# Performance work log

Measured on AMD Instinct MI355X. Metric: run time of the kernel, lower is better.

The kernel has to match this reference:

```python
import jax, jax.numpy as jnp
import numpy as np

B, N, IN, HID, OUT = 32, 128, 64, 128, 64
_off = np.ones((N, N)) - np.eye(N)
RECV, SEND = np.where(_off)  # rel_rec one-hot rows -> receiver idx, rel_send -> sender idx
E = N * (N - 1)


def _bn(x, g, b):
    # BatchNorm1d in training mode over flattened (B*M, C), eps=1e-5, biased var
    c = x.shape[-1]
    xf = x.reshape(-1, c)
    m = xf.mean(0)
    v = ((xf - m) ** 2).mean(0)
    return (((xf - m) / jnp.sqrt(v + 1e-5)) * g + b).reshape(x.shape)


def _mlp(x, W1, b1, W2, b2, g, b):
    h = jax.nn.silu(x @ W1 + b1)
    h = jax.nn.silu(h @ W2 + b2)
    return _bn(h, g, b)


def setup_inputs() -> dict:
    key = jax.random.key(0)
    ks = jax.random.split(key, 8)
    p = lambda k, s: jax.random.normal(k, s, dtype=jnp.float32) * 0.05
    return {
        "node_feature": jax.random.normal(ks[0], (B, N, IN), dtype=jnp.float32),
        "nodes_mask": jnp.ones((B, N), dtype=jnp.float32),
        "edges_mask": jnp.ones((B, E), dtype=jnp.float32),
        "eW1": p(ks[1], (2 * IN, HID)), "eb1": jnp.full((HID,), 0.1, jnp.float32),
        "eW2": p(ks[2], (HID, HID)), "eb2": jnp.full((HID,), 0.1, jnp.float32),
        "eg": jnp.ones((HID,), jnp.float32), "ebt": jnp.zeros((HID,), jnp.float32),
        "nW1": p(ks[3], (HID, HID)), "nb1": jnp.full((HID,), 0.1, jnp.float32),
        "nW2": p(ks[4], (HID, HID)), "nb2": jnp.full((HID,), 0.1, jnp.float32),
        "ng": jnp.ones((HID,), jnp.float32), "nbt": jnp.zeros((HID,), jnp.float32),
        "mW1": p(ks[5], (IN + HID, HID)), "mb1": jnp.full((HID,), 0.1, jnp.float32),
        "mW2": p(ks[6], (HID, OUT)), "mb2": jnp.full((OUT,), 0.1, jnp.float32),
        "mg": jnp.ones((OUT,), jnp.float32), "mbt": jnp.zeros((OUT,), jnp.float32),
        "t_nodes": 0, "t_edges": 0,
    }


def reference(node_feature, nodes_mask, edges_mask,
              eW1, eb1, eW2, eb2, eg, ebt,
              nW1, nb1, nW2, nb2, ng, nbt,
              mW1, mb1, mW2, mb2, mg, mbt,
              t_nodes, t_edges):
    # edge_model: rel_send/rel_rec one-hot matmuls == gathers
    senders = node_feature[:, SEND, :]    # [B,E,IN]
    receivers = node_feature[:, RECV, :]  # [B,E,IN]
    ef = jnp.concatenate([senders, receivers], axis=-1)  # [B,E,2*IN]
    # skip_first_edge_type=True, edge_types=2 -> only edge_nn[1], norm=1.0
    em = edges_mask[:, :, None]
    msg = _mlp(ef, eW1, eb1, eW2, eb2, eg, ebt) * em  # [B,E,HID]
    mij = msg / 1.0
    out = mij * em       # attention=False
    mij_m = mij * em
    # node_model: rel_rec.T matmul == scatter-sum over receivers, then / N
    incoming = jnp.zeros((B, N, HID), msg.dtype).at[:, RECV, :].add(out) / N
    incoming = _mlp(incoming, nW1, nb1, nW2, nb2, ng, nbt) * nodes_mask[:, :, None]
    nef = jnp.concatenate([node_feature, incoming], axis=-1)  # [B,N,IN+HID]
    out_node = _mlp(nef, mW1, mb1, mW2, mb2, mg, mbt) * nodes_mask[:, :, None]
    return (out_node, mij_m)
```

## Files before the change

kernel.cpp:

```cpp
#include <hip/hip_runtime.h>
#include <hip/hip_bf16.h>

#define BB    32
#define NNODE 128
#define INF   64
#define HIDF  128
#define OUTF  64
#define EE    (NNODE*(NNODE-1))
#define TILES 127
#define NBLK_EDGE (BB*TILES)
#define ROWS_E 520192.0f
#define ROWS_N 4096.0f
#define OUT0_ELEMS (BB*NNODE*OUTF)

typedef __bf16 bf16_t;
typedef __bf16 bfrag8 __attribute__((ext_vector_type(8)));
typedef __bf16 bfrag4 __attribute__((ext_vector_type(4)));
typedef float  floatx4 __attribute__((ext_vector_type(4)));

__device__ __forceinline__ float ld_g(const void* p, size_t i, int bf) {
    return bf ? (float)((const bf16_t*)p)[i] : ((const float*)p)[i];
}
__device__ __forceinline__ void st_g(void* p, size_t i, float v, int bf) {
    if (bf) ((bf16_t*)p)[i] = (bf16_t)v; else ((float*)p)[i] = v;
}
__device__ __forceinline__ void* mij_ptr(void* dout, int bf) {
    return bf ? (void*)((bf16_t*)dout + OUT0_ELEMS)
              : (void*)((float*)dout + OUT0_ELEMS);
}
__device__ __forceinline__ float silu_f(float x) {
    x = fminf(fmaxf(x, -60.f), 60.f);
    return x / (1.0f + __expf(-x));
}

__device__ __forceinline__ int swz_col(int row, int col) {
    return col ^ ((row & 15) << 3);
}

__global__ void k_detect(const unsigned int* __restrict__ eg_words,
                         int* __restrict__ flag, float* __restrict__ totE)
{
    if (threadIdx.x == 0) *flag = (eg_words[0] == 0x3F803F80u) ? 1 : 0;
    if (threadIdx.x < 256) totE[threadIdx.x] = 0.f;
}

__global__ __launch_bounds__(256)
void k_prep(const void* __restrict__ W1g, const void* __restrict__ W2g,
            bf16_t* __restrict__ Wf1, bf16_t* __restrict__ Wf2,
            const int* __restrict__ flagp)
{
    const int bf  = *flagp;
    const int idx = blockIdx.x*256 + threadIdx.x;
    const int mat = idx >> 14;
    const int e   = idx & 16383;
    const int n   = e & 127, k = e >> 7;
    const float v = ld_g(mat ? W2g : W1g, e, bf);
    const int NB = n >> 4, ln = n & 15;
    const int ks = k >> 5, q = (k >> 3) & 3, j = k & 7;
    bf16_t* dst = mat ? Wf2 : Wf1;
    dst[((((NB*4 + ks)*4 + q)*16 + ln) << 3) + j] = (bf16_t)v;
}

__global__ __launch_bounds__(256, 4)
void k_edge_mlp(const void* __restrict__ nf,
                const bf16_t* __restrict__ Wf1, const void* __restrict__ b1g,
                const bf16_t* __restrict__ Wf2, const void* __restrict__ b2g,
                void* __restrict__ dout, const int* __restrict__ flagp,
                float* __restrict__ totE)
{
    __shared__ __align__(16) bf16_t lA[128*128];
    __shared__ float sSum[128], sQ[128];
    const int bf  = *flagp;
    void* h2out = mij_ptr(dout, bf);
    const int bx   = blockIdx.x;
    const int bIdx = bx / TILES;
    const int t    = bx - bIdx*TILES;
    const int tid  = threadIdx.x;

    if (tid < 128) { sSum[tid] = 0.f; sQ[tid] = 0.f; }

    {
#pragma unroll
        for (int s = 0; s < 8; ++s) {
            const int u = tid + s*256;
            const int m = u >> 4;
            const int c = (u & 15) ^ (m & 15);
            const int eb = t*128 + m;
            const unsigned recv = ((unsigned)eb * 33027u) >> 22;
            const unsigned rr   = (unsigned)eb - recv*127u;
            const unsigned send = rr + (rr >= recv ? 1u : 0u);
            const int node = (c & 8) ? (int)recv : (int)send;
            const int coff = (c & 7) * 8;
            const size_t gi = ((size_t)(bIdx*NNODE + node))*INF + coff;
            if (bf) {
                ((uint4*)lA)[u] = *(const uint4*)((const bf16_t*)nf + gi);
            } else {
                const float4 f0 = *(const float4*)((const float*)nf + gi);
                const float4 f1 = *(const float4*)((const float*)nf + gi + 4);
                bfrag8 v;
                v[0]=(bf16_t)f0.x; v[1]=(bf16_t)f0.y; v[2]=(bf16_t)f0.z; v[3]=(bf16_t)f0.w;
                v[4]=(bf16_t)f1.x; v[5]=(bf16_t)f1.y; v[6]=(bf16_t)f1.z; v[7]=(bf16_t)f1.w;
                *(bfrag8*)(lA + (size_t)u*8) = v;
            }
        }
    }
    __syncthreads();

    const int w  = tid >> 6;
    const int L  = tid & 63;
    const int wr = w >> 1;
    const int wc = w & 1;
    const int q  = L >> 4;
    const int ln = L & 15;

    const floatx4 zero4 = {0.f, 0.f, 0.f, 0.f};
    floatx4 acc[4][4];
#pragma unroll
    for (int mt = 0; mt < 4; ++mt)
#pragma unroll
        for (int nt = 0; nt < 4; ++nt) acc[mt][nt] = zero4;

#pragma unroll
    for (int ks = 0; ks < 4; ++ks) {
        const int kk = ks*32;
        bfrag8 af[4], bv[4];
#pragma unroll
        for (int mt = 0; mt < 4; ++mt) {
            const int R = wr*64 + mt*16 + ln;
            af[mt] = *(const bfrag8*)(lA + R*128 + swz_col(R, kk + q*8));
        }
#pragma unroll
        for (int nt = 0; nt < 4; ++nt)
            bv[nt] = *(const bfrag8*)(Wf1 + ((size_t)((wc*4 + nt)*4 + ks)*64 + L)*8);
#pragma unroll
        for (int mt = 0; mt < 4; ++mt)
#pragma unroll
            for (int nt = 0; nt < 4; ++nt)
                acc[mt][nt] = __builtin_amdgcn_mfma_f32_16x16x32_bf16(
                    af[mt], bv[nt], acc[mt][nt], 0, 0, 0);
    }
    __syncthreads();

#pragma unroll
    for (int nt = 0; nt < 4; ++nt) {
        const int col = wc*64 + nt*16 + ln;
        const float bias = ld_g(b1g, col, bf);
#pragma unroll
        for (int mt = 0; mt < 4; ++mt)
#pragma unroll
            for (int r = 0; r < 4; ++r) {
                const int R = wr*64 + mt*16 + q*4 + r;
                lA[R*128 + swz_col(R, col)] = (bf16_t)silu_f(acc[mt][nt][r] + bias);
            }
    }
    __syncthreads();

#pragma unroll
    for (int mt = 0; mt < 4; ++mt)
#pragma unroll
        for (int nt = 0; nt < 4; ++nt) acc[mt][nt] = zero4;
#pragma unroll
    for (int ks = 0; ks < 4; ++ks) {
        const int kk = ks*32;
        bfrag8 af[4], bv[4];
#pragma unroll
        for (int mt = 0; mt < 4; ++mt) {
            const int R = wr*64 + mt*16 + ln;
            af[mt] = *(const bfrag8*)(lA + R*128 + swz_col(R, kk + q*8));
        }
#pragma unroll
        for (int nt = 0; nt < 4; ++nt)
            bv[nt] = *(const bfrag8*)(Wf2 + ((size_t)((wc*4 + nt)*4 + ks)*64 + L)*8);
#pragma unroll
        for (int mt = 0; mt < 4; ++mt)
#pragma unroll
            for (int nt = 0; nt < 4; ++nt)
                acc[mt][nt] = __builtin_amdgcn_mfma_f32_16x16x32_bf16(
                    af[mt], bv[nt], acc[mt][nt], 0, 0, 0);
    }

    {
        const size_t Rbase = ((size_t)bIdx*EE + (size_t)t*128) * 128;
#pragma unroll
        for (int nt = 0; nt < 4; ++nt) {
            const int col = wc*64 + nt*16 + ln;
            const float bias = ld_g(b2g, col, bf);
            float cs = 0.f, cq = 0.f;
#pragma unroll
            for (int mt = 0; mt < 4; ++mt)
#pragma unroll
                for (int r = 0; r < 4; ++r) {
                    const int R = wr*64 + mt*16 + q*4 + r;
                    const float v = silu_f(acc[mt][nt][r] + bias);
                    cs += v; cq += v*v;
                    st_g(h2out, Rbase + (size_t)R*128 + col, v, bf);
                }
            atomicAdd(&sSum[col], cs);
            atomicAdd(&sQ[col], cq);
        }
    }
    __syncthreads();
    if (tid < 128) {
        atomicAdd(&totE[tid],       sSum[tid]);
        atomicAdd(&totE[128 + tid], sQ[tid]);
    }
}

__global__ void k_finalize_edge(const float* __restrict__ tot,
                                const void* __restrict__ g,
                                const void* __restrict__ bt,
                                float* __restrict__ ab,
                                const int* __restrict__ flagp)
{
    const int bf = *flagp;
    const int c = threadIdx.x;
    const float m = tot[c] / ROWS_E;
    float v = tot[128 + c] / ROWS_E - m*m;
    v = fmaxf(v, 0.f);
    const float a = ld_g(g, c, bf) * rsqrtf(v + 1e-5f);
    ab[c]       = a;
    ab[128 + c] = ld_g(bt, c, bf) - m*a;
}

__global__ __launch_bounds__(256)
void k_bn_scatter(void* __restrict__ dout,
                  const void* __restrict__ emask,
                  const float* __restrict__ ab,
                  float* __restrict__ inc,
                  const int* __restrict__ flagp)
{
    const int bf = *flagp;
    void* h2 = mij_ptr(dout, bf);
    const int bx = blockIdx.x;
    const int b  = bx >> 7, i = bx & 127;
    const int tid = threadIdx.x;
    const int cg = tid & 31, p = tid >> 5;
    const int c0 = cg*4;
    const float al0 = ab[c0+0], al1 = ab[c0+1], al2 = ab[c0+2], al3 = ab[c0+3];
    const float be0 = ab[128+c0+0], be1 = ab[128+c0+1], be2 = ab[128+c0+2], be3 = ab[128+c0+3];
    const size_t seg = (size_t)b*EE + (size_t)i*127;
    float s0=0.f, s1=0.f, s2=0.f, s3=0.f;
    for (int e = p; e < 127; e += 8) {
        const float em  = ld_g(emask, seg + e, bf);
        const float em2 = em*em;
        const size_t base = (seg + e)*128 + c0;
        float v0, v1, v2, v3;
        if (bf) {
            const bfrag4 u = *(const bfrag4*)((const bf16_t*)h2 + base);
            v0 = (float)u[0]; v1 = (float)u[1]; v2 = (float)u[2]; v3 = (float)u[3];
        } else {
            const float4 f = *(const float4*)((const float*)h2 + base);
            v0 = f.x; v1 = f.y; v2 = f.z; v3 = f.w;
        }
        v0 = (v0*al0 + be0)*em2;
        v1 = (v1*al1 + be1)*em2;
        v2 = (v2*al2 + be2)*em2;
        v3 = (v3*al3 + be3)*em2;
        if (bf) {
            bfrag4 u; u[0]=(bf16_t)v0; u[1]=(bf16_t)v1; u[2]=(bf16_t)v2; u[3]=(bf16_t)v3;
            *(bfrag4*)((bf16_t*)h2 + base) = u;
        } else {
            float4 f; f.x=v0; f.y=v1; f.z=v2; f.w=v3;
            *(float4*)((float*)h2 + base) = f;
        }
        s0 += v0; s1 += v1; s2 += v2; s3 += v3;
    }
    __shared__ float sm[8][128];
    sm[p][c0+0] = s0; sm[p][c0+1] = s1; sm[p][c0+2] = s2; sm[p][c0+3] = s3;
    __syncthreads();
    if (tid < 128) {
        float tsum = 0.f;
#pragma unroll
        for (int wk = 0; wk < 8; ++wk) tsum += sm[wk][tid];
        inc[(size_t)(b*NNODE + i)*HIDF + tid] = tsum * (1.0f/NNODE);
    }
}

__global__ __launch_bounds__(128)
void k_node_mlp(const float* __restrict__ inc,
                const void* __restrict__ W1g, const void* __restrict__ b1g,
                const void* __restrict__ W2g, const void* __restrict__ b2g,
                float* __restrict__ h2n, float* __restrict__ partialN,
                const int* __restrict__ flagp)
{
    const int bf = *flagp;
    __shared__ float x[16][128];
    __shared__ float h[16][128];
    const int bx = blockIdx.x;
    const int tid = threadIdx.x;
    const int r0 = bx*16;
    for (int r = 0; r < 16; ++r) x[r][tid] = inc[(size_t)(r0 + r)*128 + tid];
    __syncthreads();

    float a1[16];
#pragma unroll
    for (int r = 0; r < 16; ++r) a1[r] = 0.f;
#pragma unroll 4
    for (int k = 0; k < 128; ++k) {
        const float wv = ld_g(W1g, k*128 + tid, bf);
#pragma unroll
        for (int r = 0; r < 16; ++r) a1[r] += x[r][k]*wv;
    }
    const float bias1 = ld_g(b1g, tid, bf);
#pragma unroll
    for (int r = 0; r < 16; ++r) h[r][tid] = silu_f(a1[r] + bias1);
    __syncthreads();

    float a2[16];
#pragma unroll
    for (int r = 0; r < 16; ++r) a2[r] = 0.f;
#pragma unroll 4
    for (int k = 0; k < 128; ++k) {
        const float wv = ld_g(W2g, k*128 + tid, bf);
#pragma unroll
        for (int r = 0; r < 16; ++r) a2[r] += h[r][k]*wv;
    }
    const float bias2 = ld_g(b2g, tid, bf);
    float s = 0.f, sq = 0.f;
#pragma unroll
    for (int r = 0; r < 16; ++r) {
        const float v = silu_f(a2[r] + bias2);
        h2n[(size_t)(r0 + r)*128 + tid] = v;
        s += v; sq += v*v;
    }
    partialN[(size_t)bx*256 + tid]       = s;
    partialN[(size_t)bx*256 + 128 + tid] = sq;
}

__global__ void k_finalize_node(const float* __restrict__ p,
                                const void* __restrict__ g,
                                const void* __restrict__ bt,
                                float* __restrict__ ab,
                                const int* __restrict__ flagp)
{
    const int bf = *flagp;
    const int c = threadIdx.x;
    float s = 0.f, qv = 0.f;
#pragma unroll 8
    for (int blk = 0; blk < 256; ++blk) { s += p[blk*256 + c]; qv += p[blk*256 + 128 + c]; }
    const float m = s / ROWS_N;
    float v = qv / ROWS_N - m*m;
    v = fmaxf(v, 0.f);
    const float a = ld_g(g, c, bf) * rsqrtf(v + 1e-5f);
    ab[c]       = a;
    ab[128 + c] = ld_g(bt, c, bf) - m*a;
}

__global__ __launch_bounds__(128)
void k_final_mlp(const void* __restrict__ nf,
                 const float* __restrict__ h2n, const float* __restrict__ abn,
                 const void* __restrict__ nmask,
                 const void* __restrict__ W1g, const void* __restrict__ b1g,
                 const void* __restrict__ W2g, const void* __restrict__ b2g,
                 float* __restrict__ hm, float* __restrict__ partialM,
                 const int* __restrict__ flagp)
{
    const int bf = *flagp;
    __shared__ float x[16][192];
    __shared__ float h[16][128];
    const int bx = blockIdx.x;
    const int tid = threadIdx.x;
    const int r0 = bx*16;
    const float an = abn[tid], bn = abn[128 + tid];
    for (int r = 0; r < 16; ++r) {
        const int row = r0 + r;
        const float mask = ld_g(nmask, row, bf);
        if (tid < 64) x[r][tid] = ld_g(nf, (size_t)row*INF + tid, bf);
        x[r][64 + tid] = (h2n[(size_t)row*128 + tid]*an + bn) * mask;
    }
    __syncthreads();

    float a1[16];
#pragma unroll
    for (int r = 0; r < 16; ++r) a1[r] = 0.f;
#pragma unroll 4
    for (int k = 0; k < 192; ++k) {
        const float wv = ld_g(W1g, k*128 + tid, bf);
#pragma unroll
        for (int r = 0; r < 16; ++r) a1[r] += x[r][k]*wv;
    }
    const float bias1 = ld_g(b1g, tid, bf);
#pragma unroll
    for (int r = 0; r < 16; ++r) h[r][tid] = silu_f(a1[r] + bias1);
    __syncthreads();

    if (tid < 64) {
        float a2[16];
#pragma unroll
        for (int r = 0; r < 16; ++r) a2[r] = 0.f;
#pragma unroll 4
        for (int k = 0; k < 128; ++k) {
            const float wv = ld_g(W2g, k*64 + tid, bf);
#pragma unroll
            for (int r = 0; r < 16; ++r) a2[r] += h[r][k]*wv;
        }
        const float bias2 = ld_g(b2g, tid, bf);
        float s = 0.f, sq = 0.f;
#pragma unroll
        for (int r = 0; r < 16; ++r) {
            const float v = silu_f(a2[r] + bias2);
            hm[(size_t)(r0 + r)*OUTF + tid] = v;
            s += v; sq += v*v;
        }
        partialM[(size_t)bx*128 + tid]      = s;
        partialM[(size_t)bx*128 + 64 + tid] = sq;
    }
}

__global__ void k_finalize_m(const float* __restrict__ p,
                             const void* __restrict__ g,
                             const void* __restrict__ bt,
                             float* __restrict__ ab,
                             const int* __restrict__ flagp)
{
    const int bf = *flagp;
    const int c = threadIdx.x;
    float s = 0.f, qv = 0.f;
#pragma unroll 8
    for (int blk = 0; blk < 256; ++blk) { s += p[blk*128 + c]; qv += p[blk*128 + 64 + c]; }
    const float m = s / ROWS_N;
    float v = qv / ROWS_N - m*m;
    v = fmaxf(v, 0.f);
    const float a = ld_g(g, c, bf) * rsqrtf(v + 1e-5f);
    ab[c]      = a;
    ab[64 + c] = ld_g(bt, c, bf) - m*a;
}

__global__ void k_out_node(const float* __restrict__ hm,
                           const float* __restrict__ abm,
                           const void* __restrict__ nmask,
                           void* __restrict__ dout,
                           const int* __restrict__ flagp)
{
    const int bf = *flagp;
    const int idx = blockIdx.x*256 + threadIdx.x;
    if (idx >= OUT0_ELEMS) return;
    const int c = idx & 63;
    const int row = idx >> 6;
    const float v = (hm[idx]*abm[c] + abm[64 + c]) * ld_g(nmask, row, bf);
    st_g(dout, idx, v, bf);
}

extern "C" void kernel_launch(void* const* d_in, const int* in_sizes, int n_in,
                              void* d_out, int out_size, void* d_ws, size_t ws_size,
                              hipStream_t stream)
{
    const void* nf    = d_in[0];
    const void* nmask = d_in[1];
    const void* emask = d_in[2];
    const void* eW1   = d_in[3];
    const void* eb1   = d_in[4];
    const void* eW2   = d_in[5];
    const void* eb2   = d_in[6];
    const void* eg    = d_in[7];
    const void* ebt   = d_in[8];
    const void* nW1   = d_in[9];
    const void* nb1   = d_in[10];
    const void* nW2   = d_in[11];
    const void* nb2   = d_in[12];
    const void* ng    = d_in[13];
    const void* nbt   = d_in[14];
    const void* mW1   = d_in[15];
    const void* mb1   = d_in[16];
    const void* mW2   = d_in[17];
    const void* mb2   = d_in[18];
    const void* mg    = d_in[19];
    const void* mbt   = d_in[20];

    float* W    = (float*)d_ws;
    int*   flag = (int*)W;
    float* totE = W    + 64;
    float* abE  = totE + 256;
    float* inc  = abE  + 256;
    float* h2n  = inc  + 524288;
    float* pN   = h2n  + 524288;
    float* abN  = pN   + 65536;
    float* hm   = abN  + 256;
    float* pM   = hm   + 262144;
    float* abM  = pM   + 32768;
    bf16_t* Wf1 = (bf16_t*)(abM + 128);
    bf16_t* Wf2 = Wf1 + 16384;

    k_detect<<<dim3(1), dim3(256), 0, stream>>>((const unsigned int*)eg, flag, totE);
    k_prep<<<dim3(128), dim3(256), 0, stream>>>(eW1, eW2, Wf1, Wf2, flag);
    k_edge_mlp<<<dim3(NBLK_EDGE), dim3(256), 0, stream>>>(nf, Wf1, eb1, Wf2, eb2, d_out, flag, totE);
    k_finalize_edge<<<dim3(1), dim3(128), 0, stream>>>(totE, eg, ebt, abE, flag);
    k_bn_scatter<<<dim3(BB*NNODE), dim3(256), 0, stream>>>(d_out, emask, abE, inc, flag);
    k_node_mlp<<<dim3(256), dim3(128), 0, stream>>>(inc, nW1, nb1, nW2, nb2, h2n, pN, flag);
    k_finalize_node<<<dim3(1), dim3(128), 0, stream>>>(pN, ng, nbt, abN, flag);
    k_final_mlp<<<dim3(256), dim3(128), 0, stream>>>(nf, h2n, abN, nmask, mW1, mb1, mW2, mb2, hm, pM, flag);
    k_finalize_m<<<dim3(1), dim3(64), 0, stream>>>(pM, mg, mbt, abM, flag);
    k_out_node<<<dim3(1024), dim3(256), 0, stream>>>(hm, abM, nmask, d_out, flag);
}
```

Baseline: 653.2 us.

## Stage edge MLP output through LDS as bf16 for coalesced stores

The edge MLP epilogue now writes SiLU outputs into shared memory as bf16, reduces the per-column BN statistics with wave shuffles before the LDS atomics, then streams the whole tile to global memory with 16-byte coalesced stores. When the workspace is large enough, the pre-BN activations go to a bf16 scratch buffer so the fp32 path writes and rereads half the bytes. The BN/scatter kernel reads and writes 8 channels per thread. SiLU drops its clamp and uses a fast reciprocal, and the node MLP loops unroll further. Rounding the pre-BN values to bf16 in fp32 mode adds precision loss.

```diff
diff --git a/kernel.cpp b/kernel.cpp
--- a/kernel.cpp
+++ b/kernel.cpp
@@ -12,6 +12,7 @@
 #define ROWS_E 520192.0f
 #define ROWS_N 4096.0f
 #define OUT0_ELEMS (BB*NNODE*OUTF)
+#define H2_ELEMS ((size_t)520192*128)
 
 typedef __bf16 bf16_t;
 typedef __bf16 bfrag8 __attribute__((ext_vector_type(8)));
@@ -29,8 +30,7 @@
               : (void*)((float*)dout + OUT0_ELEMS);
 }
 __device__ __forceinline__ float silu_f(float x) {
-    x = fminf(fmaxf(x, -60.f), 60.f);
-    return x / (1.0f + __expf(-x));
+    return x * __builtin_amdgcn_rcpf(1.0f + __expf(-x));
 }
 
 __device__ __forceinline__ int swz_col(int row, int col) {
@@ -65,8 +65,9 @@
 void k_edge_mlp(const void* __restrict__ nf,
                 const bf16_t* __restrict__ Wf1, const void* __restrict__ b1g,
                 const bf16_t* __restrict__ Wf2, const void* __restrict__ b2g,
-                void* __restrict__ dout, const int* __restrict__ flagp,
-                float* __restrict__ totE)
+                void* __restrict__ dout, bf16_t* __restrict__ h2ws,
+                const int* __restrict__ flagp, float* __restrict__ totE,
+                int h2mode)
 {
     __shared__ __align__(16) bf16_t lA[128*128];
     __shared__ float sSum[128], sQ[128];
@@ -178,31 +179,53 @@
                 acc[mt][nt] = __builtin_amdgcn_mfma_f32_16x16x32_bf16(
                     af[mt], bv[nt], acc[mt][nt], 0, 0, 0);
     }
+    __syncthreads();
+
+#pragma unroll
+    for (int nt = 0; nt < 4; ++nt) {
+        const int col = wc*64 + nt*16 + ln;
+        const float bias = ld_g(b2g, col, bf);
+        float cs = 0.f, cq = 0.f;
+#pragma unroll
+        for (int mt = 0; mt < 4; ++mt)
+#pragma unroll
+            for (int r = 0; r < 4; ++r) {
+                const int R = wr*64 + mt*16 + q*4 + r;
+                const float v = silu_f(acc[mt][nt][r] + bias);
+                cs += v; cq += v*v;
+                lA[R*128 + swz_col(R, col)] = (bf16_t)v;
+            }
+        cs += __shfl_xor(cs, 16); cs += __shfl_xor(cs, 32);
+        cq += __shfl_xor(cq, 16); cq += __shfl_xor(cq, 32);
+        if (L < 16) { atomicAdd(&sSum[col], cs); atomicAdd(&sQ[col], cq); }
+    }
+    __syncthreads();
 
     {
         const size_t Rbase = ((size_t)bIdx*EE + (size_t)t*128) * 128;
 #pragma unroll
-        for (int nt = 0; nt < 4; ++nt) {
-            const int col = wc*64 + nt*16 + ln;
-            const float bias = ld_g(b2g, col, bf);
-            float cs = 0.f, cq = 0.f;
-#pragma unroll
-            for (int mt = 0; mt < 4; ++mt)
-#pragma unroll
-                for (int r = 0; r < 4; ++r) {
-                    const int R = wr*64 + mt*16 + q*4 + r;
-                    const float v = silu_f(acc[mt][nt][r] + bias);
-                    cs += v; cq += v*v;
-                    st_g(h2out, Rbase + (size_t)R*128 + col, v, bf);
-                }
-            atomicAdd(&sSum[col], cs);
-            atomicAdd(&sQ[col], cq);
-        }
-    }
-    __syncthreads();
-    if (tid < 128) {
-        atomicAdd(&totE[tid],       sSum[tid]);
-        atomicAdd(&totE[128 + tid], sQ[tid]);
+        for (int s = 0; s < 8; ++s) {
+            const int u = tid + s*256;
+            const int m = u >> 4;
+            const int c = (u & 15) ^ (m & 15);
+            const size_t go = Rbase + (size_t)m*128 + c*8;
+            if (h2mode) {
+                *(uint4*)(h2ws + go) = ((const uint4*)lA)[u];
+            } else if (bf) {
+                *(uint4*)((bf16_t*)h2out + go) = ((const uint4*)lA)[u];
+            } else {
+                const bfrag8 vv = *(const bfrag8*)(lA + (size_t)u*8);
+                float4 f0, f1;
+                f0.x=(float)vv[0]; f0.y=(float)vv[1]; f0.z=(float)vv[2]; f0.w=(float)vv[3];
+                f1.x=(float)vv[4]; f1.y=(float)vv[5]; f1.z=(float)vv[6]; f1.w=(float)vv[7];
+                *(float4*)((float*)h2out + go)     = f0;
+                *(float4*)((float*)h2out + go + 4) = f1;
+            }
+        }
+        if (tid < 128) {
+            atomicAdd(&totE[tid],       sSum[tid]);
+            atomicAdd(&totE[128 + tid], sQ[tid]);
+        }
     }
 }
 
@@ -224,54 +247,66 @@
 
 __global__ __launch_bounds__(256)
 void k_bn_scatter(void* __restrict__ dout,
+                  const bf16_t* __restrict__ h2ws,
                   const void* __restrict__ emask,
                   const float* __restrict__ ab,
                   float* __restrict__ inc,
-                  const int* __restrict__ flagp)
-{
-    const int bf = *flagp;
-    void* h2 = mij_ptr(dout, bf);
+                  const int* __restrict__ flagp, int h2mode)
+{
+    const int bf = *flagp;
+    void* mij = mij_ptr(dout, bf);
+    const void* h2 = h2mode ? (const void*)h2ws : (const void*)mij;
+    const int h2bf = h2mode | bf;
     const int bx = blockIdx.x;
     const int b  = bx >> 7, i = bx & 127;
     const int tid = threadIdx.x;
-    const int cg = tid & 31, p = tid >> 5;
-    const int c0 = cg*4;
-    const float al0 = ab[c0+0], al1 = ab[c0+1], al2 = ab[c0+2], al3 = ab[c0+3];
-    const float be0 = ab[128+c0+0], be1 = ab[128+c0+1], be2 = ab[128+c0+2], be3 = ab[128+c0+3];
+    const int cg = tid & 15, p = tid >> 4;
+    const int c0 = cg*8;
+    float al[8], be[8];
+#pragma unroll
+    for (int j = 0; j < 8; ++j) { al[j] = ab[c0+j]; be[j] = ab[128+c0+j]; }
     const size_t seg = (size_t)b*EE + (size_t)i*127;
-    float s0=0.f, s1=0.f, s2=0.f, s3=0.f;
-    for (int e = p; e < 127; e += 8) {
+    float s[8];
+#pragma unroll
+    for (int j = 0; j < 8; ++j) s[j] = 0.f;
+    for (int e = p; e < 127; e += 16) {
         const float em  = ld_g(emask, seg + e, bf);
         const float em2 = em*em;
         const size_t base = (seg + e)*128 + c0;
-        float v0, v1, v2, v3;
+        float v[8];
+        if (h2bf) {
+            const bfrag8 u = *(const bfrag8*)((const bf16_t*)h2 + base);
+#pragma unroll
+            for (int j = 0; j < 8; ++j) v[j] = (float)u[j];
+        } else {
+            const float4 f0 = *(const float4*)((const float*)h2 + base);
+            const float4 f1 = *(const float4*)((const float*)h2 + base + 4);
+            v[0]=f0.x; v[1]=f0.y; v[2]=f0.z; v[3]=f0.w;
+            v[4]=f1.x; v[5]=f1.y; v[6]=f1.z; v[7]=f1.w;
+        }
+#pragma unroll
+        for (int j = 0; j < 8; ++j) { v[j] = (v[j]*al[j] + be[j])*em2; s[j] += v[j]; }
         if (bf) {
-            const bfrag4 u = *(const bfrag4*)((const bf16_t*)h2 + base);
-            v0 = (float)u[0]; v1 = (float)u[1]; v2 = (float)u[2]; v3 = (float)u[3];
+            bfrag8 u;
+#pragma unroll
+            for (int j = 0; j < 8; ++j) u[j] = (bf16_t)v[j];
+            *(bfrag8*)((bf16_t*)mij + base) = u;
         } else {
-            const float4 f = *(const float4*)((const float*)h2 + base);
-            v0 = f.x; v1 = f.y; v2 = f.z; v3 = f.w;
-        }
-        v0 = (v0*al0 + be0)*em2;
-        v1 = (v1*al1 + be1)*em2;
-        v2 = (v2*al2 + be2)*em2;
-        v3 = (v3*al3 + be3)*em2;
-        if (bf) {
-            bfrag4 u; u[0]=(bf16_t)v0; u[1]=(bf16_t)v1; u[2]=(bf16_t)v2; u[3]=(bf16_t)v3;
-            *(bfrag4*)((bf16_t*)h2 + base) = u;
-        } else {
-            float4 f; f.x=v0; f.y=v1; f.z=v2; f.w=v3;
-            *(float4*)((float*)h2 + base) = f;
-        }
-        s0 += v0; s1 += v1; s2 += v2; s3 += v3;
-    }
-    __shared__ float sm[8][128];
-    sm[p][c0+0] = s0; sm[p][c0+1] = s1; sm[p][c0+2] = s2; sm[p][c0+3] = s3;
+            float4 f0, f1;
+            f0.x=v[0]; f0.y=v[1]; f0.z=v[2]; f0.w=v[3];
+            f1.x=v[4]; f1.y=v[5]; f1.z=v[6]; f1.w=v[7];
+            *(float4*)((float*)mij + base)     = f0;
+            *(float4*)((float*)mij + base + 4) = f1;
+        }
+    }
+    __shared__ float sm[16][128];
+#pragma unroll
+    for (int j = 0; j < 8; ++j) sm[p][c0+j] = s[j];
     __syncthreads();
     if (tid < 128) {
         float tsum = 0.f;
 #pragma unroll
-        for (int wk = 0; wk < 8; ++wk) tsum += sm[wk][tid];
+        for (int wk = 0; wk < 16; ++wk) tsum += sm[wk][tid];
         inc[(size_t)(b*NNODE + i)*HIDF + tid] = tsum * (1.0f/NNODE);
     }
 }
@@ -295,7 +330,7 @@
     float a1[16];
 #pragma unroll
     for (int r = 0; r < 16; ++r) a1[r] = 0.f;
-#pragma unroll 4
+#pragma unroll 8
     for (int k = 0; k < 128; ++k) {
         const float wv = ld_g(W1g, k*128 + tid, bf);
 #pragma unroll
@@ -309,7 +344,7 @@
     float a2[16];
 #pragma unroll
     for (int r = 0; r < 16; ++r) a2[r] = 0.f;
-#pragma unroll 4
+#pragma unroll 8
     for (int k = 0; k < 128; ++k) {
         const float wv = ld_g(W2g, k*128 + tid, bf);
 #pragma unroll
@@ -373,7 +408,7 @@
     float a1[16];
 #pragma unroll
     for (int r = 0; r < 16; ++r) a1[r] = 0.f;
-#pragma unroll 4
+#pragma unroll 8
     for (int k = 0; k < 192; ++k) {
         const float wv = ld_g(W1g, k*128 + tid, bf);
 #pragma unroll
@@ -388,7 +423,7 @@
         float a2[16];
 #pragma unroll
         for (int r = 0; r < 16; ++r) a2[r] = 0.f;
-#pragma unroll 4
+#pragma unroll 8
         for (int k = 0; k < 128; ++k) {
             const float wv = ld_g(W2g, k*64 + tid, bf);
 #pragma unroll
@@ -480,12 +515,16 @@
     float* abM  = pM   + 32768;
     bf16_t* Wf1 = (bf16_t*)(abM + 128);
     bf16_t* Wf2 = Wf1 + 16384;
+    bf16_t* h2ws = Wf2 + 16384;
+
+    const size_t base_bytes = (size_t)((char*)h2ws - (char*)d_ws);
+    const int h2mode = (ws_size >= base_bytes + H2_ELEMS*2 + 256) ? 1 : 0;
 
     k_detect<<<dim3(1), dim3(256), 0, stream>>>((const unsigned int*)eg, flag, totE);
     k_prep<<<dim3(128), dim3(256), 0, stream>>>(eW1, eW2, Wf1, Wf2, flag);
-    k_edge_mlp<<<dim3(NBLK_EDGE), dim3(256), 0, stream>>>(nf, Wf1, eb1, Wf2, eb2, d_out, flag, totE);
+    k_edge_mlp<<<dim3(NBLK_EDGE), dim3(256), 0, stream>>>(nf, Wf1, eb1, Wf2, eb2, d_out, h2ws, flag, totE, h2mode);
     k_finalize_edge<<<dim3(1), dim3(128), 0, stream>>>(totE, eg, ebt, abE, flag);
-    k_bn_scatter<<<dim3(BB*NNODE), dim3(256), 0, stream>>>(d_out, emask, abE, inc, flag);
+    k_bn_scatter<<<dim3(BB*NNODE), dim3(256), 0, stream>>>(d_out, h2ws, emask, abE, inc, flag, h2mode);
     k_node_mlp<<<dim3(256), dim3(128), 0, stream>>>(inc, nW1, nb1, nW2, nb2, h2n, pN, flag);
     k_finalize_node<<<dim3(1), dim3(128), 0, stream>>>(pN, ng, nbt, abN, flag);
     k_final_mlp<<<dim3(256), dim3(128), 0, stream>>>(nf, h2n, abN, nmask, mW1, mb1, mW2, mb2, hm, pM, flag);
```

Result: faster. 630.6 us (-3.5%).
